# Kernel optimization log

Hardware: AMD Instinct MI355X
Metric: run time of the kernel (lower is better)

The kernel has to match this reference:

```python
import jax, jax.numpy as jnp
import numpy as np

DIM = 512
HEADS = 8
DIM_HEAD = 64
INNER = HEADS * DIM_HEAD
SCALE = DIM_HEAD ** -0.5


def setup_inputs() -> dict:
    key = jax.random.key(0)
    k1, k2, k3, k4 = jax.random.split(key, 4)
    x = jax.random.normal(k1, (2, 4096, DIM), dtype=jnp.float32)
    # torch Linear stores weight [out, in]; we keep [in, out] for x @ W
    W_qkv = jax.random.normal(k2, (DIM, 3 * INNER), dtype=jnp.float32) * (DIM ** -0.5)
    W_out = jax.random.normal(k3, (INNER, DIM), dtype=jnp.float32) * (INNER ** -0.5)
    b_out = jax.random.normal(k4, (DIM,), dtype=jnp.float32) * 0.01
    return {"x": x, "W_qkv": W_qkv, "W_out": W_out, "b_out": b_out}


def reference(x, W_qkv, W_out, b_out):
    b, l, _ = x.shape
    qkv = x @ W_qkv  # [b, l, 3*inner]
    q, k, v = jnp.split(qkv, 3, axis=-1)

    def split_heads(t):  # [b, l, inner] -> [b, h, l, d]
        return t.reshape(b, l, HEADS, DIM_HEAD).transpose(0, 2, 1, 3)

    q, k, v = split_heads(q), split_heads(k), split_heads(v)
    attn = jnp.einsum('bhid,bhjd->bhij', q, k) * SCALE
    attn = jax.nn.softmax(attn, axis=-1)
    attned = jnp.einsum('bhij,bhjd->bhid', attn, v)
    attned = attned.transpose(0, 2, 1, 3).reshape(b, l, INNER)
    return attned @ W_out + b_out
```

## Files before the change

### kernel.cpp

```cpp
#include <hip/hip_runtime.h>

typedef short bf16x8 __attribute__((ext_vector_type(8)));
typedef float f32x4 __attribute__((ext_vector_type(4)));

#define MFMA16(a, b, c) __builtin_amdgcn_mfma_f32_16x16x32_bf16((a), (b), (c), 0, 0, 0)

__device__ __forceinline__ unsigned short f2bf(float f) {
    union { float f; unsigned u; } v; v.f = f;
    unsigned r = v.u + 0x7FFFu + ((v.u >> 16) & 1u);
    return (unsigned short)(r >> 16);
}

__global__ __launch_bounds__(256) void k_cvt(const float* __restrict__ in,
                                             unsigned short* __restrict__ out, int n4) {
    int i = blockIdx.x * 256 + threadIdx.x;
    if (i < n4) {
        float4 v = reinterpret_cast<const float4*>(in)[i];
        ushort4 o;
        o.x = f2bf(v.x); o.y = f2bf(v.y); o.z = f2bf(v.z); o.w = f2bf(v.w);
        reinterpret_cast<ushort4*>(out)[i] = o;
    }
}

__global__ __launch_bounds__(256) void k_tr(const float* __restrict__ in,
                                            unsigned short* __restrict__ out, int R, int C) {
    __shared__ float t[64][65];
    int c0 = blockIdx.x * 64, r0 = blockIdx.y * 64;
    int lc = threadIdx.x & 63, lr4 = threadIdx.x >> 6;
#pragma unroll
    for (int j = 0; j < 16; ++j) {
        int r = lr4 + j * 4;
        t[r][lc] = in[(size_t)(r0 + r) * C + c0 + lc];
    }
    __syncthreads();
#pragma unroll
    for (int j = 0; j < 16; ++j) {
        int c = lr4 + j * 4;
        out[(size_t)(c0 + c) * R + r0 + lc] = f2bf(t[lc][c]);
    }
}

__device__ __forceinline__ void gemm_main_512(const unsigned short* __restrict__ A,
                                              const unsigned short* __restrict__ Bt,
                                              int m0, int n0,
                                              unsigned short* AL, unsigned short* BL,
                                              f32x4 acc[4][4]) {
    const int tid = threadIdx.x;
    const int lane = tid & 63, wid = tid >> 6;
    const int wr = wid >> 1, wc = wid & 1;
    const int lg = lane >> 4, lr = lane & 15;

    for (int k0 = 0; k0 < 512; k0 += 32) {
#pragma unroll
        for (int i = 0; i < 2; ++i) {
            int idx = tid + i * 256;
            int row = idx >> 2;
            int c8 = (idx & 3) * 8;
            *reinterpret_cast<bf16x8*>(&AL[row * 40 + c8]) =
                *reinterpret_cast<const bf16x8*>(&A[(size_t)(m0 + row) * 512 + k0 + c8]);
            *reinterpret_cast<bf16x8*>(&BL[row * 40 + c8]) =
                *reinterpret_cast<const bf16x8*>(&Bt[(size_t)(n0 + row) * 512 + k0 + c8]);
        }
        __syncthreads();
        bf16x8 af[4], bfr[4];
#pragma unroll
        for (int rt = 0; rt < 4; ++rt)
            af[rt] = *reinterpret_cast<const bf16x8*>(&AL[(wr * 64 + rt * 16 + lr) * 40 + lg * 8]);
#pragma unroll
        for (int ct = 0; ct < 4; ++ct)
            bfr[ct] = *reinterpret_cast<const bf16x8*>(&BL[(wc * 64 + ct * 16 + lr) * 40 + lg * 8]);
#pragma unroll
        for (int rt = 0; rt < 4; ++rt)
#pragma unroll
            for (int ct = 0; ct < 4; ++ct)
                acc[rt][ct] = MFMA16(af[rt], bfr[ct], acc[rt][ct]);
        __syncthreads();
    }
}

__global__ __launch_bounds__(256) void k_gemm_qkv(const unsigned short* __restrict__ X,
                                                  const unsigned short* __restrict__ Wt,
                                                  unsigned short* __restrict__ Qb,
                                                  unsigned short* __restrict__ Kb,
                                                  unsigned short* __restrict__ VbT) {
    __shared__ __align__(16) unsigned short AL[128 * 40];
    __shared__ __align__(16) unsigned short BL[128 * 40];
    f32x4 acc[4][4];
#pragma unroll
    for (int i = 0; i < 4; ++i)
#pragma unroll
        for (int j = 0; j < 4; ++j) acc[i][j] = (f32x4){0.f, 0.f, 0.f, 0.f};

    int m0 = blockIdx.x * 128, n0 = blockIdx.y * 128;
    gemm_main_512(X, Wt, m0, n0, AL, BL, acc);

    const int tid = threadIdx.x;
    const int lane = tid & 63, wid = tid >> 6;
    const int wr = wid >> 1, wc = wid & 1;
    const int lg = lane >> 4, lr = lane & 15;
#pragma unroll
    for (int rt = 0; rt < 4; ++rt) {
#pragma unroll
        for (int ct = 0; ct < 4; ++ct) {
            int col = n0 + wc * 64 + ct * 16 + lr;
            int which = col >> 9, inner = col & 511;
            int h = inner >> 6, d = inner & 63;
#pragma unroll
            for (int j = 0; j < 4; ++j) {
                int row = m0 + wr * 64 + rt * 16 + lg * 4 + j;
                int b = row >> 12, l = row & 4095;
                float v = acc[rt][ct][j];
                if (which == 0) {
                    Qb[(((size_t)(b * 8 + h)) * 4096 + l) * 64 + d] = f2bf(v * 0.18033688f);
                } else if (which == 1) {
                    Kb[(((size_t)(b * 8 + h)) * 4096 + l) * 64 + d] = f2bf(v);
                } else {
                    VbT[(((size_t)(b * 8 + h)) * 64 + d) * 4096 + l] = f2bf(v);
                }
            }
        }
    }
}

__global__ __launch_bounds__(256) void k_gemm_out(const unsigned short* __restrict__ An,
                                                  const unsigned short* __restrict__ Wot,
                                                  const float* __restrict__ bout,
                                                  float* __restrict__ out) {
    __shared__ __align__(16) unsigned short AL[128 * 40];
    __shared__ __align__(16) unsigned short BL[128 * 40];
    f32x4 acc[4][4];
#pragma unroll
    for (int i = 0; i < 4; ++i)
#pragma unroll
        for (int j = 0; j < 4; ++j) acc[i][j] = (f32x4){0.f, 0.f, 0.f, 0.f};

    int m0 = blockIdx.x * 128, n0 = blockIdx.y * 128;
    gemm_main_512(An, Wot, m0, n0, AL, BL, acc);

    const int tid = threadIdx.x;
    const int lane = tid & 63, wid = tid >> 6;
    const int wr = wid >> 1, wc = wid & 1;
    const int lg = lane >> 4, lr = lane & 15;
#pragma unroll
    for (int rt = 0; rt < 4; ++rt) {
#pragma unroll
        for (int ct = 0; ct < 4; ++ct) {
            int col = n0 + wc * 64 + ct * 16 + lr;
            float bv = bout[col];
#pragma unroll
            for (int j = 0; j < 4; ++j) {
                int row = m0 + wr * 64 + rt * 16 + lg * 4 + j;
                out[(size_t)row * 512 + col] = acc[rt][ct][j] + bv;
            }
        }
    }
}

__global__ __launch_bounds__(256) void k_attn(const unsigned short* __restrict__ Q,
                                              const unsigned short* __restrict__ K,
                                              const unsigned short* __restrict__ VT,
                                              unsigned short* __restrict__ O) {
    __shared__ __align__(16) unsigned short KL[64 * 72];
    __shared__ __align__(16) unsigned short VTl[64 * 72];
    __shared__ __align__(16) unsigned short PL[4][32 * 72];

    const int qt = blockIdx.x;
    const int bh = blockIdx.y;
    const size_t base = (size_t)bh * 4096 * 64;
    const int tid = threadIdx.x, lane = tid & 63, wid = tid >> 6;
    const int lg = lane >> 4, lr = lane & 15;
    const int q0 = qt * 128 + wid * 32;

    bf16x8 qf[2][2];
#pragma unroll
    for (int rt = 0; rt < 2; ++rt)
#pragma unroll
        for (int kt = 0; kt < 2; ++kt)
            qf[rt][kt] = *reinterpret_cast<const bf16x8*>(
                &Q[base + (size_t)(q0 + rt * 16 + lr) * 64 + kt * 32 + lg * 8]);

    f32x4 oacc[2][4];
    f32x4 sacc[2];
#pragma unroll
    for (int rt = 0; rt < 2; ++rt) {
        sacc[rt] = (f32x4){0.f, 0.f, 0.f, 0.f};
#pragma unroll
        for (int dt = 0; dt < 4; ++dt) oacc[rt][dt] = (f32x4){0.f, 0.f, 0.f, 0.f};
    }

    bf16x8 ones;
#pragma unroll
    for (int j = 0; j < 8; ++j) ones[j] = (short)0x3F80;

    const int r0 = tid >> 3, c0 = (tid & 7) * 8;

    bf16x8 kreg[2], vreg[2];
#pragma unroll
    for (int i = 0; i < 2; ++i) {
        kreg[i] = *reinterpret_cast<const bf16x8*>(&K[base + (size_t)(r0 + i * 32) * 64 + c0]);
        vreg[i] = *reinterpret_cast<const bf16x8*>(&VT[base + (size_t)(r0 + i * 32) * 4096 + c0]);
    }
#pragma unroll
    for (int i = 0; i < 2; ++i) {
        *reinterpret_cast<bf16x8*>(&KL[(r0 + i * 32) * 72 + c0]) = kreg[i];
        *reinterpret_cast<bf16x8*>(&VTl[(r0 + i * 32) * 72 + c0]) = vreg[i];
    }
    __syncthreads();

    for (int kv = 0; kv < 64; ++kv) {
        const int kv0n = kv * 64 + 64;
        if (kv < 63) {
#pragma unroll
            for (int i = 0; i < 2; ++i) {
                kreg[i] = *reinterpret_cast<const bf16x8*>(
                    &K[base + (size_t)(kv0n + r0 + i * 32) * 64 + c0]);
                vreg[i] = *reinterpret_cast<const bf16x8*>(
                    &VT[base + (size_t)(r0 + i * 32) * 4096 + kv0n + c0]);
            }
        }

        f32x4 s[2][4];
#pragma unroll
        for (int rt = 0; rt < 2; ++rt)
#pragma unroll
            for (int ct = 0; ct < 4; ++ct) s[rt][ct] = (f32x4){0.f, 0.f, 0.f, 0.f};
#pragma unroll
        for (int kt = 0; kt < 2; ++kt) {
#pragma unroll
            for (int ct = 0; ct < 4; ++ct) {
                bf16x8 kf = *reinterpret_cast<const bf16x8*>(
                    &KL[(ct * 16 + lr) * 72 + kt * 32 + lg * 8]);
#pragma unroll
                for (int rt = 0; rt < 2; ++rt)
                    s[rt][ct] = MFMA16(qf[rt][kt], kf, s[rt][ct]);
            }
        }

#pragma unroll
        for (int rt = 0; rt < 2; ++rt)
#pragma unroll
            for (int ct = 0; ct < 4; ++ct)
#pragma unroll
                for (int j = 0; j < 4; ++j)
                    PL[wid][(rt * 16 + lg * 4 + j) * 72 + ct * 16 + lr] =
                        f2bf(__builtin_amdgcn_exp2f(s[rt][ct][j]));

#pragma unroll
        for (int kt = 0; kt < 2; ++kt) {
            bf16x8 pf[2];
#pragma unroll
            for (int rt = 0; rt < 2; ++rt)
                pf[rt] = *reinterpret_cast<const bf16x8*>(
                    &PL[wid][(rt * 16 + lr) * 72 + kt * 32 + lg * 8]);
#pragma unroll
            for (int dt = 0; dt < 4; ++dt) {
                bf16x8 vf = *reinterpret_cast<const bf16x8*>(
                    &VTl[(dt * 16 + lr) * 72 + kt * 32 + lg * 8]);
#pragma unroll
                for (int rt = 0; rt < 2; ++rt)
                    oacc[rt][dt] = MFMA16(pf[rt], vf, oacc[rt][dt]);
            }
#pragma unroll
            for (int rt = 0; rt < 2; ++rt)
                sacc[rt] = MFMA16(pf[rt], ones, sacc[rt]);
        }

        __syncthreads();
        if (kv < 63) {
#pragma unroll
            for (int i = 0; i < 2; ++i) {
                *reinterpret_cast<bf16x8*>(&KL[(r0 + i * 32) * 72 + c0]) = kreg[i];
                *reinterpret_cast<bf16x8*>(&VTl[(r0 + i * 32) * 72 + c0]) = vreg[i];
            }
        }
        __syncthreads();
    }

    const int b = bh >> 3, h = bh & 7;
#pragma unroll
    for (int rt = 0; rt < 2; ++rt) {
#pragma unroll
        for (int j = 0; j < 4; ++j) {
            float inv = 1.f / sacc[rt][j];
            int row = q0 + rt * 16 + lg * 4 + j;
#pragma unroll
            for (int dt = 0; dt < 4; ++dt) {
                int d = dt * 16 + lr;
                O[((size_t)b * 4096 + row) * 512 + h * 64 + d] = f2bf(oacc[rt][dt][j] * inv);
            }
        }
    }
}

extern "C" void kernel_launch(void* const* d_in, const int* in_sizes, int n_in,
                              void* d_out, int out_size, void* d_ws, size_t ws_size,
                              hipStream_t stream) {
    const float* x    = (const float*)d_in[0];
    const float* Wqkv = (const float*)d_in[1];
    const float* Wout = (const float*)d_in[2];
    const float* bout = (const float*)d_in[3];
    float* out = (float*)d_out;

    char* ws = (char*)d_ws;
    unsigned short* Xbf  = (unsigned short*)(ws);
    unsigned short* Wqkt = (unsigned short*)(ws + 8388608);
    unsigned short* Wot  = (unsigned short*)(ws + 8388608 + 1572864);
    unsigned short* Qb   = (unsigned short*)(ws + 10485760);
    unsigned short* Kb   = (unsigned short*)(ws + 18874368);
    unsigned short* VbT  = (unsigned short*)(ws + 27262976);
    unsigned short* An   = (unsigned short*)(ws + 35651584);

    k_cvt<<<4096, 256, 0, stream>>>(x, Xbf, 4194304 / 4);
    k_tr<<<dim3(24, 8), 256, 0, stream>>>(Wqkv, Wqkt, 512, 1536);
    k_tr<<<dim3(8, 8), 256, 0, stream>>>(Wout, Wot, 512, 512);
    k_gemm_qkv<<<dim3(64, 12), 256, 0, stream>>>(Xbf, Wqkt, Qb, Kb, VbT);
    k_attn<<<dim3(32, 16), 256, 0, stream>>>(Qb, Kb, VbT, An);
    k_gemm_out<<<dim3(64, 4), 256, 0, stream>>>(An, Wot, bout, out);
}
```

Measured before the change: 232.5 us.

## Split attention KV range across two blocks and combine with a reduction kernel

The attention grid gains a third dimension that splits the 4096 keys into two halves. Each block writes an unnormalised partial output and its row sums, and a new reduce kernel adds the two partials and divides by the summed denominators. The goal is to double the number of attention blocks so the GPU is better filled. The cost is an extra launch, about 24 MB of extra partial-result traffic, and rounding the partials to bf16 before they are combined. The change also raises wave priority around the MFMA sections with s_setprio and packs the transposed V stores in the QKV epilogue into ushort4 writes.

```diff
diff --git a/kernel.cpp b/kernel.cpp
--- a/kernel.cpp
+++ b/kernel.cpp
@@ -9,6 +9,10 @@
     union { float f; unsigned u; } v; v.f = f;
     unsigned r = v.u + 0x7FFFu + ((v.u >> 16) & 1u);
     return (unsigned short)(r >> 16);
+}
+__device__ __forceinline__ float bf2f(unsigned short s) {
+    union { unsigned u; float f; } v; v.u = (unsigned)s << 16;
+    return v.f;
 }
 
 __global__ __launch_bounds__(256) void k_cvt(const float* __restrict__ in,
@@ -98,25 +102,31 @@
     const int lane = tid & 63, wid = tid >> 6;
     const int wr = wid >> 1, wc = wid & 1;
     const int lg = lane >> 4, lr = lane & 15;
+    const int which = n0 >> 9;
 #pragma unroll
     for (int rt = 0; rt < 4; ++rt) {
 #pragma unroll
         for (int ct = 0; ct < 4; ++ct) {
             int col = n0 + wc * 64 + ct * 16 + lr;
-            int which = col >> 9, inner = col & 511;
+            int inner = col & 511;
             int h = inner >> 6, d = inner & 63;
-#pragma unroll
-            for (int j = 0; j < 4; ++j) {
-                int row = m0 + wr * 64 + rt * 16 + lg * 4 + j;
-                int b = row >> 12, l = row & 4095;
-                float v = acc[rt][ct][j];
-                if (which == 0) {
-                    Qb[(((size_t)(b * 8 + h)) * 4096 + l) * 64 + d] = f2bf(v * 0.18033688f);
-                } else if (which == 1) {
-                    Kb[(((size_t)(b * 8 + h)) * 4096 + l) * 64 + d] = f2bf(v);
-                } else {
-                    VbT[(((size_t)(b * 8 + h)) * 64 + d) * 4096 + l] = f2bf(v);
-                }
+            int row0 = m0 + wr * 64 + rt * 16 + lg * 4;
+            int b = row0 >> 12, l0 = row0 & 4095;
+            if (which == 0) {
+#pragma unroll
+                for (int j = 0; j < 4; ++j)
+                    Qb[(((size_t)(b * 8 + h)) * 4096 + l0 + j) * 64 + d] =
+                        f2bf(acc[rt][ct][j] * 0.18033688f);
+            } else if (which == 1) {
+#pragma unroll
+                for (int j = 0; j < 4; ++j)
+                    Kb[(((size_t)(b * 8 + h)) * 4096 + l0 + j) * 64 + d] = f2bf(acc[rt][ct][j]);
+            } else {
+                ushort4 o;
+                o.x = f2bf(acc[rt][ct][0]); o.y = f2bf(acc[rt][ct][1]);
+                o.z = f2bf(acc[rt][ct][2]); o.w = f2bf(acc[rt][ct][3]);
+                *reinterpret_cast<ushort4*>(
+                    &VbT[(((size_t)(b * 8 + h)) * 64 + d) * 4096 + l0]) = o;
             }
         }
     }
@@ -159,14 +169,18 @@
 __global__ __launch_bounds__(256) void k_attn(const unsigned short* __restrict__ Q,
                                               const unsigned short* __restrict__ K,
                                               const unsigned short* __restrict__ VT,
-                                              unsigned short* __restrict__ O) {
+                                              unsigned short* __restrict__ Op0,
+                                              unsigned short* __restrict__ Op1,
+                                              float* __restrict__ Lp) {
     __shared__ __align__(16) unsigned short KL[64 * 72];
     __shared__ __align__(16) unsigned short VTl[64 * 72];
     __shared__ __align__(16) unsigned short PL[4][32 * 72];
 
     const int qt = blockIdx.x;
     const int bh = blockIdx.y;
+    const int hh = blockIdx.z;
     const size_t base = (size_t)bh * 4096 * 64;
+    const int kvbase = hh * 2048;
     const int tid = threadIdx.x, lane = tid & 63, wid = tid >> 6;
     const int lg = lane >> 4, lr = lane & 15;
     const int q0 = qt * 128 + wid * 32;
@@ -197,8 +211,10 @@
     bf16x8 kreg[2], vreg[2];
 #pragma unroll
     for (int i = 0; i < 2; ++i) {
-        kreg[i] = *reinterpret_cast<const bf16x8*>(&K[base + (size_t)(r0 + i * 32) * 64 + c0]);
-        vreg[i] = *reinterpret_cast<const bf16x8*>(&VT[base + (size_t)(r0 + i * 32) * 4096 + c0]);
+        kreg[i] = *reinterpret_cast<const bf16x8*>(
+            &K[base + (size_t)(kvbase + r0 + i * 32) * 64 + c0]);
+        vreg[i] = *reinterpret_cast<const bf16x8*>(
+            &VT[base + (size_t)(r0 + i * 32) * 4096 + kvbase + c0]);
     }
 #pragma unroll
     for (int i = 0; i < 2; ++i) {
@@ -207,9 +223,9 @@
     }
     __syncthreads();
 
-    for (int kv = 0; kv < 64; ++kv) {
-        const int kv0n = kv * 64 + 64;
-        if (kv < 63) {
+    for (int kv = 0; kv < 32; ++kv) {
+        const int kv0n = kvbase + kv * 64 + 64;
+        if (kv < 31) {
 #pragma unroll
             for (int i = 0; i < 2; ++i) {
                 kreg[i] = *reinterpret_cast<const bf16x8*>(
@@ -224,6 +240,7 @@
         for (int rt = 0; rt < 2; ++rt)
 #pragma unroll
             for (int ct = 0; ct < 4; ++ct) s[rt][ct] = (f32x4){0.f, 0.f, 0.f, 0.f};
+        __builtin_amdgcn_s_setprio(1);
 #pragma unroll
         for (int kt = 0; kt < 2; ++kt) {
 #pragma unroll
@@ -235,6 +252,7 @@
                     s[rt][ct] = MFMA16(qf[rt][kt], kf, s[rt][ct]);
             }
         }
+        __builtin_amdgcn_s_setprio(0);
 
 #pragma unroll
         for (int rt = 0; rt < 2; ++rt)
@@ -245,6 +263,7 @@
                     PL[wid][(rt * 16 + lg * 4 + j) * 72 + ct * 16 + lr] =
                         f2bf(__builtin_amdgcn_exp2f(s[rt][ct][j]));
 
+        __builtin_amdgcn_s_setprio(1);
 #pragma unroll
         for (int kt = 0; kt < 2; ++kt) {
             bf16x8 pf[2];
@@ -264,9 +283,10 @@
             for (int rt = 0; rt < 2; ++rt)
                 sacc[rt] = MFMA16(pf[rt], ones, sacc[rt]);
         }
+        __builtin_amdgcn_s_setprio(0);
 
         __syncthreads();
-        if (kv < 63) {
+        if (kv < 31) {
 #pragma unroll
             for (int i = 0; i < 2; ++i) {
                 *reinterpret_cast<bf16x8*>(&KL[(r0 + i * 32) * 72 + c0]) = kreg[i];
@@ -276,20 +296,43 @@
         __syncthreads();
     }
 
+    unsigned short* Op = hh ? Op1 : Op0;
     const int b = bh >> 3, h = bh & 7;
 #pragma unroll
     for (int rt = 0; rt < 2; ++rt) {
 #pragma unroll
         for (int j = 0; j < 4; ++j) {
-            float inv = 1.f / sacc[rt][j];
             int row = q0 + rt * 16 + lg * 4 + j;
 #pragma unroll
             for (int dt = 0; dt < 4; ++dt) {
                 int d = dt * 16 + lr;
-                O[((size_t)b * 4096 + row) * 512 + h * 64 + d] = f2bf(oacc[rt][dt][j] * inv);
-            }
-        }
-    }
+                Op[((size_t)b * 4096 + row) * 512 + h * 64 + d] = f2bf(oacc[rt][dt][j]);
+            }
+            if (lr == 0)
+                Lp[((size_t)(hh * 16 + bh)) * 4096 + row] = sacc[rt][j];
+        }
+    }
+}
+
+__global__ __launch_bounds__(256) void k_reduce(const unsigned short* __restrict__ O0,
+                                                const unsigned short* __restrict__ O1,
+                                                const float* __restrict__ Lp,
+                                                unsigned short* __restrict__ An) {
+    int i4 = blockIdx.x * 256 + threadIdx.x;
+    int e = i4 * 4;
+    int r = e >> 9;
+    int c = e & 511, h = c >> 6;
+    int b = r >> 12, l = r & 4095;
+    int lidx = (b * 8 + h) * 4096 + l;
+    float inv = 1.f / (Lp[lidx] + Lp[16 * 4096 + lidx]);
+    ushort4 a = *reinterpret_cast<const ushort4*>(&O0[e]);
+    ushort4 bq = *reinterpret_cast<const ushort4*>(&O1[e]);
+    ushort4 o;
+    o.x = f2bf((bf2f(a.x) + bf2f(bq.x)) * inv);
+    o.y = f2bf((bf2f(a.y) + bf2f(bq.y)) * inv);
+    o.z = f2bf((bf2f(a.z) + bf2f(bq.z)) * inv);
+    o.w = f2bf((bf2f(a.w) + bf2f(bq.w)) * inv);
+    *reinterpret_cast<ushort4*>(&An[e]) = o;
 }
 
 extern "C" void kernel_launch(void* const* d_in, const int* in_sizes, int n_in,
@@ -309,11 +352,15 @@
     unsigned short* Kb   = (unsigned short*)(ws + 18874368);
     unsigned short* VbT  = (unsigned short*)(ws + 27262976);
     unsigned short* An   = (unsigned short*)(ws + 35651584);
+    unsigned short* Op0  = Xbf;
+    unsigned short* Op1  = An;
+    float*          Lp   = (float*)(ws + 8388608);
 
     k_cvt<<<4096, 256, 0, stream>>>(x, Xbf, 4194304 / 4);
     k_tr<<<dim3(24, 8), 256, 0, stream>>>(Wqkv, Wqkt, 512, 1536);
     k_tr<<<dim3(8, 8), 256, 0, stream>>>(Wout, Wot, 512, 512);
     k_gemm_qkv<<<dim3(64, 12), 256, 0, stream>>>(Xbf, Wqkt, Qb, Kb, VbT);
-    k_attn<<<dim3(32, 16), 256, 0, stream>>>(Qb, Kb, VbT, An);
+    k_attn<<<dim3(32, 16, 2), 256, 0, stream>>>(Qb, Kb, VbT, Op0, Op1, Lp);
+    k_reduce<<<4096, 256, 0, stream>>>(Op0, Op1, Lp, An);
     k_gemm_out<<<dim3(64, 4), 256, 0, stream>>>(An, Wot, bout, out);
 }
```

Measured after the change: 239.1 us. 2.8% more time.
